# Performance work log

Measured on AMD Instinct MI355X. Metric: run time of the kernel, lower is better.

Reference implementation:

```python
import jax, jax.numpy as jnp
import numpy as np


def _rot_x(a):  # a: [N], angle = theta[:,1]
    c, s = jnp.cos(a), jnp.sin(a)
    z, o = jnp.zeros_like(c), jnp.ones_like(c)
    return jnp.stack([
        jnp.stack([o, z, z, z], -1),
        jnp.stack([z, c, -s, z], -1),
        jnp.stack([z, s, c, z], -1),
        jnp.stack([z, z, z, o], -1)], axis=1)  # [N,4,4]


def _rot_y(a):  # angle = theta[:,0]
    c, s = jnp.cos(a), jnp.sin(a)
    z, o = jnp.zeros_like(c), jnp.ones_like(c)
    return jnp.stack([
        jnp.stack([c, z, s, z], -1),
        jnp.stack([z, o, z, z], -1),
        jnp.stack([-s, z, c, z], -1),
        jnp.stack([z, z, z, o], -1)], axis=1)


def _rot_z(a):  # angle = theta[:,2]
    c, s = jnp.cos(a), jnp.sin(a)
    z, o = jnp.zeros_like(c), jnp.ones_like(c)
    return jnp.stack([
        jnp.stack([c, -s, z, z], -1),
        jnp.stack([s, c, z, z], -1),
        jnp.stack([z, z, o, z], -1),
        jnp.stack([z, z, z, o], -1)], axis=1)


def _trans(th):  # th: [N,6] -> [N,3,4] affine translation matrix
    tx, ty, tz = th[:, 3], th[:, 4], th[:, 5]
    z, o = jnp.zeros_like(tx), jnp.ones_like(tx)
    return jnp.stack([
        jnp.stack([o, z, z, tx], -1),
        jnp.stack([z, o, z, ty], -1),
        jnp.stack([z, z, o, tz], -1)], axis=1)  # [N,3,4]


def _homogeneous(x_flat, J):
    # x_flat: [N, 3*J] -> [N, 4, J] homogeneous coords (joints as columns)
    N = x_flat.shape[0]
    pts = x_flat.reshape(N, J, 3).transpose(0, 2, 1)  # [N,3,J]
    ones = jnp.ones((N, 1, J), dtype=x_flat.dtype)
    return jnp.concatenate([pts, ones], axis=1)  # [N,4,J]


def va_forward(conv_input, theta):
    B, T, D = conv_input.shape
    J = D // 3
    th = theta.reshape(-1, theta.shape[-1])  # [N,6], N = B*T
    mask = (conv_input != 0.0).astype(conv_input.dtype)  # [B,T,D]

    # translation: out = Trans @ hom(x)
    hom = _homogeneous(conv_input.reshape(-1, D), J)  # [N,4,J]
    out = jnp.einsum('nij,njk->nik', _trans(th), hom)  # [N,3,J]
    out = out.transpose(0, 2, 1).reshape(B, T, D)
    out = out * mask

    # rotation: M = Rz @ Ry @ Rx
    M = jnp.einsum('nij,njk->nik', _rot_z(th[:, 2]), _rot_y(th[:, 0]))
    M = jnp.einsum('nij,njk->nik', M, _rot_x(th[:, 1]))  # [N,4,4]
    hom2 = _homogeneous(out.reshape(-1, D), J)  # [N,4,J]
    out2 = jnp.einsum('nij,njk->nik', M, hom2)  # [N,4,J]
    out2 = out2.transpose(0, 2, 1)[:, :, 0:3]  # [N,J,3]
    return out2.reshape(B, T, D)


def setup_inputs() -> dict:
    key = jax.random.key(0)
    k1, k2 = jax.random.split(key)
    conv_input = jax.random.normal(k1, (2048, 300, 75), dtype=jnp.float32)
    theta = jax.random.normal(k2, (2048, 300, 6), dtype=jnp.float32)
    return {"conv_input": conv_input, "theta": theta}


def reference(conv_input, theta):
    return va_forward(conv_input, theta)
```

## Files before the change

kernel.cpp:

```cpp
#include <hip/hip_runtime.h>


constexpr int JOINTS          = 25;
constexpr int FLOATS_PER_ROW  = 75;
constexpr int ROWS_PER_BLOCK  = 32;
constexpr int BLOCK           = 256;
constexpr int FLOATS_PER_BLK  = ROWS_PER_BLOCK * FLOATS_PER_ROW;
constexpr int VEC4_PER_BLK    = FLOATS_PER_BLK / 4;
constexpr int TASKS_PER_BLK   = ROWS_PER_BLOCK * JOINTS;

__global__ __launch_bounds__(BLOCK) void va_kernel(
    const float4* __restrict__ conv4,
    const float*  __restrict__ theta,
    float4*       __restrict__ out4,
    int nrows)
{
    __shared__ float buf[FLOATS_PER_BLK];
    __shared__ float prm[ROWS_PER_BLOCK][12];

    const int tid = threadIdx.x;
    const size_t row0  = (size_t)blockIdx.x * ROWS_PER_BLOCK;
    const size_t base4 = (size_t)blockIdx.x * VEC4_PER_BLK;
    const size_t total4 = (size_t)nrows * FLOATS_PER_ROW / 4;

    #pragma unroll
    for (int i = tid; i < VEC4_PER_BLK; i += BLOCK) {
        size_t g = base4 + i;
        if (g < total4)
            *reinterpret_cast<float4*>(&buf[i * 4]) = conv4[g];
    }

    if (tid < ROWS_PER_BLOCK) {
        size_t row = row0 + tid;
        if (row < (size_t)nrows) {
            const float* th = theta + row * 6;
            float ay = th[0], ax = th[1], az = th[2];
            float tx = th[3], ty = th[4], tz = th[5];

            float sy = __sinf(ay), cy = __cosf(ay);
            float sx = __sinf(ax), cx = __cosf(ax);
            float sz = __sinf(az), cz = __cosf(az);

            prm[tid][0] = cz * cy;
            prm[tid][1] = -sz * cx + cz * sy * sx;
            prm[tid][2] =  sz * sx + cz * sy * cx;
            prm[tid][3] = sz * cy;
            prm[tid][4] =  cz * cx + sz * sy * sx;
            prm[tid][5] = -cz * sx + sz * sy * cx;
            prm[tid][6] = -sy;
            prm[tid][7] = cy * sx;
            prm[tid][8] = cy * cx;
            prm[tid][9]  = tx;
            prm[tid][10] = ty;
            prm[tid][11] = tz;
        }
    }
    __syncthreads();

    #pragma unroll
    for (int t = tid; t < TASKS_PER_BLK; t += BLOCK) {
        int r = t / JOINTS;
        float* p = &buf[3 * t];
        const float* m = prm[r];

        float x = p[0], y = p[1], z = p[2];
        float qx = (x != 0.0f) ? (x + m[9])  : 0.0f;
        float qy = (y != 0.0f) ? (y + m[10]) : 0.0f;
        float qz = (z != 0.0f) ? (z + m[11]) : 0.0f;

        p[0] = m[0] * qx + m[1] * qy + m[2] * qz;
        p[1] = m[3] * qx + m[4] * qy + m[5] * qz;
        p[2] = m[6] * qx + m[7] * qy + m[8] * qz;
    }
    __syncthreads();

    #pragma unroll
    for (int i = tid; i < VEC4_PER_BLK; i += BLOCK) {
        size_t g = base4 + i;
        if (g < total4)
            out4[g] = *reinterpret_cast<const float4*>(&buf[i * 4]);
    }
}

extern "C" void kernel_launch(void* const* d_in, const int* in_sizes, int n_in,
                              void* d_out, int out_size, void* d_ws, size_t ws_size,
                              hipStream_t stream) {
    const float4* conv4 = (const float4*)d_in[0];
    const float*  theta = (const float*)d_in[1];
    float4* out4 = (float4*)d_out;

    int nrows  = out_size / FLOATS_PER_ROW;
    int blocks = (nrows + ROWS_PER_BLOCK - 1) / ROWS_PER_BLOCK;
    va_kernel<<<blocks, BLOCK, 0, stream>>>(conv4, theta, out4, nrows);
}
```

Baseline: 77.91 us.

## Write outputs directly from compute loop, drop bounds checks and second sync

The rotated results are now stored straight to global memory as scalar stride-3 writes instead of going back to shared memory, then through a barrier, then out as float4. The theta load is hoisted ahead of the input staging loop so its latency overlaps with it. All tail bounds checks are removed and the grid is sized as nrows/32, which assumes the row count divides evenly by 32 (600 blocks' worth here does). Scalar stride-3 stores are less coalesced than float4 stores, so store efficiency may drop.

```diff
diff --git a/kernel.cpp b/kernel.cpp
--- a/kernel.cpp
+++ b/kernel.cpp
@@ -12,8 +12,7 @@
 __global__ __launch_bounds__(BLOCK) void va_kernel(
     const float4* __restrict__ conv4,
     const float*  __restrict__ theta,
-    float4*       __restrict__ out4,
-    int nrows)
+    float*        __restrict__ out)
 {
     __shared__ float buf[FLOATS_PER_BLK];
     __shared__ float prm[ROWS_PER_BLOCK][12];
@@ -21,64 +20,60 @@
     const int tid = threadIdx.x;
     const size_t row0  = (size_t)blockIdx.x * ROWS_PER_BLOCK;
     const size_t base4 = (size_t)blockIdx.x * VEC4_PER_BLK;
-    const size_t total4 = (size_t)nrows * FLOATS_PER_ROW / 4;
+
+    float ay, ax, az, tx, ty, tz;
+    if (tid < ROWS_PER_BLOCK) {
+        const float* th = theta + (row0 + tid) * 6;
+        ay = th[0]; ax = th[1]; az = th[2];
+        tx = th[3]; ty = th[4]; tz = th[5];
+    }
 
     #pragma unroll
-    for (int i = tid; i < VEC4_PER_BLK; i += BLOCK) {
-        size_t g = base4 + i;
-        if (g < total4)
-            *reinterpret_cast<float4*>(&buf[i * 4]) = conv4[g];
+    for (int k = 0; k < 3; ++k) {
+        int i = tid + k * BLOCK;
+        if (i < VEC4_PER_BLK)
+            *reinterpret_cast<float4*>(&buf[i * 4]) = conv4[base4 + i];
     }
 
     if (tid < ROWS_PER_BLOCK) {
-        size_t row = row0 + tid;
-        if (row < (size_t)nrows) {
-            const float* th = theta + row * 6;
-            float ay = th[0], ax = th[1], az = th[2];
-            float tx = th[3], ty = th[4], tz = th[5];
+        float sy = __sinf(ay), cy = __cosf(ay);
+        float sx = __sinf(ax), cx = __cosf(ax);
+        float sz = __sinf(az), cz = __cosf(az);
 
-            float sy = __sinf(ay), cy = __cosf(ay);
-            float sx = __sinf(ax), cx = __cosf(ax);
-            float sz = __sinf(az), cz = __cosf(az);
-
-            prm[tid][0] = cz * cy;
-            prm[tid][1] = -sz * cx + cz * sy * sx;
-            prm[tid][2] =  sz * sx + cz * sy * cx;
-            prm[tid][3] = sz * cy;
-            prm[tid][4] =  cz * cx + sz * sy * sx;
-            prm[tid][5] = -cz * sx + sz * sy * cx;
-            prm[tid][6] = -sy;
-            prm[tid][7] = cy * sx;
-            prm[tid][8] = cy * cx;
-            prm[tid][9]  = tx;
-            prm[tid][10] = ty;
-            prm[tid][11] = tz;
-        }
+        prm[tid][0] = cz * cy;
+        prm[tid][1] = -sz * cx + cz * sy * sx;
+        prm[tid][2] =  sz * sx + cz * sy * cx;
+        prm[tid][3] = sz * cy;
+        prm[tid][4] =  cz * cx + sz * sy * sx;
+        prm[tid][5] = -cz * sx + sz * sy * cx;
+        prm[tid][6] = -sy;
+        prm[tid][7] = cy * sx;
+        prm[tid][8] = cy * cx;
+        prm[tid][9]  = tx;
+        prm[tid][10] = ty;
+        prm[tid][11] = tz;
     }
     __syncthreads();
 
+    float* oblk = out + base4 * 4;
     #pragma unroll
-    for (int t = tid; t < TASKS_PER_BLK; t += BLOCK) {
-        int r = t / JOINTS;
-        float* p = &buf[3 * t];
-        const float* m = prm[r];
+    for (int k = 0; k < 4; ++k) {
+        int t = tid + k * BLOCK;
+        if (t < TASKS_PER_BLK) {
+            int r = t / JOINTS;
+            const float* p = &buf[3 * t];
+            const float* m = prm[r];
 
-        float x = p[0], y = p[1], z = p[2];
-        float qx = (x != 0.0f) ? (x + m[9])  : 0.0f;
-        float qy = (y != 0.0f) ? (y + m[10]) : 0.0f;
-        float qz = (z != 0.0f) ? (z + m[11]) : 0.0f;
+            float x = p[0], y = p[1], z = p[2];
+            float qx = (x != 0.0f) ? (x + m[9])  : 0.0f;
+            float qy = (y != 0.0f) ? (y + m[10]) : 0.0f;
+            float qz = (z != 0.0f) ? (z + m[11]) : 0.0f;
 
-        p[0] = m[0] * qx + m[1] * qy + m[2] * qz;
-        p[1] = m[3] * qx + m[4] * qy + m[5] * qz;
-        p[2] = m[6] * qx + m[7] * qy + m[8] * qz;
-    }
-    __syncthreads();
-
-    #pragma unroll
-    for (int i = tid; i < VEC4_PER_BLK; i += BLOCK) {
-        size_t g = base4 + i;
-        if (g < total4)
-            out4[g] = *reinterpret_cast<const float4*>(&buf[i * 4]);
+            float* o = oblk + 3 * t;
+            o[0] = m[0] * qx + m[1] * qy + m[2] * qz;
+            o[1] = m[3] * qx + m[4] * qy + m[5] * qz;
+            o[2] = m[6] * qx + m[7] * qy + m[8] * qz;
+        }
     }
 }
 
@@ -87,9 +82,9 @@
                               hipStream_t stream) {
     const float4* conv4 = (const float4*)d_in[0];
     const float*  theta = (const float*)d_in[1];
-    float4* out4 = (float4*)d_out;
+    float* out = (float*)d_out;
 
     int nrows  = out_size / FLOATS_PER_ROW;
-    int blocks = (nrows + ROWS_PER_BLOCK - 1) / ROWS_PER_BLOCK;
-    va_kernel<<<blocks, BLOCK, 0, stream>>>(conv4, theta, out4, nrows);
+    int blocks = nrows / ROWS_PER_BLOCK;
+    va_kernel<<<blocks, BLOCK, 0, stream>>>(conv4, theta, out);
 }
```

Result: faster. 74.94 us (-3.8%).
